# Optimization experiments

Hardware: AMD Instinct MI355X
Metric: run time of the kernel (lower is better)

## Reference

```python
import jax, jax.numpy as jnp
import numpy as np

N = 100000      # nodes
E = 1600000     # edges
D = 64          # in_dim (node/edge feature dim)
H = 128         # hidden = 2*in_dim (num_layers=2 MLP)
OUT = 64        # out_dim
EPS = 1e-7      # GENConv eps
BN_EPS = 1e-5   # BatchNorm1d eps
NORM_EPS = 1e-12  # F.normalize eps


def setup_inputs() -> dict:
    key = jax.random.key(0)
    ks = jax.random.split(key, 10)
    feats = jax.random.normal(ks[0], (N, D), dtype=jnp.float32)
    edge_h = jax.random.normal(ks[1], (E, D), dtype=jnp.float32)
    src = jax.random.randint(ks[2], (E,), 0, N, dtype=jnp.int32)
    dst = jax.random.randint(ks[3], (E,), 0, N, dtype=jnp.int32)
    # MLP params: Linear(D,H) -> BN(H) -> ReLU -> Linear(H,OUT)
    W1 = jax.random.normal(ks[4], (D, H), dtype=jnp.float32) * 0.05
    b1 = jnp.zeros((H,), dtype=jnp.float32)
    gamma = jnp.ones((H,), dtype=jnp.float32)
    bn_beta = jnp.zeros((H,), dtype=jnp.float32)
    W2 = jax.random.normal(ks[5], (H, OUT), dtype=jnp.float32) * 0.05
    b2 = jnp.zeros((OUT,), dtype=jnp.float32)
    scale = jnp.ones((1,), dtype=jnp.float32)  # MessageNorm scale (not learned)
    return {"feats": feats, "edge_h": edge_h, "src": src, "dst": dst,
            "W1": W1, "b1": b1, "gamma": gamma, "bn_beta": bn_beta,
            "W2": W2, "b2": b2, "scale": scale}


def reference(feats, edge_h, W1, b1, gamma, bn_beta, W2, b2, scale, src, dst):
    beta = 1.0
    # message: m = relu(x_src + e) + eps            [E, D]
    m = jax.nn.relu(feats[src] + edge_h) + EPS
    # edge_softmax over incoming edges of each dst node (per feature channel)
    logits = m * beta
    gmax = jax.ops.segment_max(logits, dst, num_segments=N)   # [N, D]
    ex = jnp.exp(logits - gmax[dst])                          # [E, D]
    den = jax.ops.segment_sum(ex, dst, num_segments=N)        # [N, D]
    a = ex / den[dst]
    # weighted scatter-sum aggregation
    h = jax.ops.segment_sum(m * a, dst, num_segments=N)       # [N, D]
    # MessageNorm: feats + normalize(msg) * ||feats||_2 * scale
    feat_norm = jnp.linalg.norm(feats, axis=-1, keepdims=True)
    msg_norm = jnp.linalg.norm(h, axis=-1, keepdims=True)
    msg = h / jnp.maximum(msg_norm, NORM_EPS)
    x = feats + msg * feat_norm * scale
    # MLP: Linear -> BatchNorm1d (training-mode batch stats) -> ReLU -> Linear
    x = x @ W1 + b1
    mean = jnp.mean(x, axis=0)
    var = jnp.mean(jnp.square(x - mean), axis=0)  # biased, as torch BN
    x = (x - mean) * jax.lax.rsqrt(var + BN_EPS) * gamma + bn_beta
    x = jax.nn.relu(x)
    return x @ W2 + b2
```

## Files before the change

### kernel.cpp

```cpp
#include <hip/hip_runtime.h>
#include <cstdint>

#define N_NODES 100000
#define E_EDGES 1600000
#define D_IN 64
#define H_DIM 128
#define OUT_DIM 64
#define EPS_GEN 1e-7f
#define BN_EPS 1e-5f
#define NORM_EPS 1e-12f

__global__ __launch_bounds__(256) void hist_kernel(
    const int* __restrict__ dst, int* __restrict__ counts)
{
    int t = blockIdx.x * 256 + threadIdx.x;
    if (t < E_EDGES / 4) {
        int4 d = ((const int4*)dst)[t];
        atomicAdd(&counts[d.x], 1);
        atomicAdd(&counts[d.y], 1);
        atomicAdd(&counts[d.z], 1);
        atomicAdd(&counts[d.w], 1);
    }
}

__global__ __launch_bounds__(256) void scan1(
    const int* __restrict__ counts, int* __restrict__ row_start,
    int* __restrict__ bsum)
{
    __shared__ int s[256];
    int t = threadIdx.x, g = blockIdx.x * 256 + t;
    int v = (g < N_NODES) ? counts[g] : 0;
    s[t] = v;
    __syncthreads();
    #pragma unroll
    for (int off = 1; off < 256; off <<= 1) {
        int u = (t >= off) ? s[t - off] : 0;
        __syncthreads();
        s[t] += u;
        __syncthreads();
    }
    if (g < N_NODES) row_start[g] = s[t];
    if (t == 255) bsum[blockIdx.x] = s[255];
}

__global__ __launch_bounds__(512) void scan2(int* __restrict__ bsum, int nb)
{
    __shared__ int s[512];
    int t = threadIdx.x;
    int v = (t < nb) ? bsum[t] : 0;
    s[t] = v;
    __syncthreads();
    #pragma unroll
    for (int off = 1; off < 512; off <<= 1) {
        int u = (t >= off) ? s[t - off] : 0;
        __syncthreads();
        s[t] += u;
        __syncthreads();
    }
    if (t < nb) bsum[t] = s[t] - v;
}

__global__ __launch_bounds__(256) void scan3(
    const int* __restrict__ counts, const int* __restrict__ bsum,
    int* __restrict__ row_start, int* __restrict__ next)
{
    int g = blockIdx.x * 256 + threadIdx.x;
    if (g < N_NODES) {
        int incl = row_start[g];
        int rs = incl - counts[g] + bsum[blockIdx.x];
        row_start[g] = rs;
        next[g] = rs;
    }
    if (g == 0) row_start[N_NODES] = E_EDGES;
}

__global__ __launch_bounds__(256) void scatter_k(
    const int* __restrict__ dst, const int* __restrict__ src,
    int* __restrict__ next, int2* __restrict__ adj)
{
    int t = blockIdx.x * 256 + threadIdx.x;
    if (t < E_EDGES / 4) {
        int4 d = ((const int4*)dst)[t];
        int4 s = ((const int4*)src)[t];
        int e0 = 4 * t;
        int p0 = atomicAdd(&next[d.x], 1);
        adj[p0] = make_int2(e0 + 0, s.x);
        int p1 = atomicAdd(&next[d.y], 1);
        adj[p1] = make_int2(e0 + 1, s.y);
        int p2 = atomicAdd(&next[d.z], 1);
        adj[p2] = make_int2(e0 + 2, s.z);
        int p3 = atomicAdd(&next[d.w], 1);
        adj[p3] = make_int2(e0 + 3, s.w);
    }
}

__global__ __launch_bounds__(256) void aggregate(
    const float* __restrict__ feats, const float* __restrict__ edge_h,
    const int2* __restrict__ adj, const int* __restrict__ row_start,
    const float* __restrict__ scale, float* __restrict__ x)
{
    int node = blockIdx.x * 4 + (threadIdx.x >> 6);
    int lane = threadIdx.x & 63;
    if (node >= N_NODES) return;
    int rs = row_start[node], re = row_start[node + 1];
    float den = 0.f, hn = 0.f;

    for (int base = rs; base < re; base += 64) {
        int rem = min(64, re - base);
        int2 ad = (base + lane < re) ? adj[base + lane] : make_int2(0, 0);
        for (int j = 0; j < rem; j += 8) {
            #pragma unroll
            for (int u = 0; u < 8; u++) {
                int jj = j + u;
                int eid = __shfl(ad.x, jj);
                int sid = __shfl(ad.y, jj);
                float fv = feats[(size_t)sid * D_IN + lane];
                float ev = __builtin_nontemporal_load(
                               &edge_h[(size_t)eid * D_IN + lane]);
                float m = fmaxf(fv + ev, 0.f) + EPS_GEN;
                float ex = __expf(m);
                bool ok = jj < rem;
                den += ok ? ex : 0.f;
                hn  += ok ? m * ex : 0.f;
            }
        }
    }

    float h = den > 0.f ? hn / den : 0.f;
    float f = feats[(size_t)node * D_IN + lane];
    float s1 = h * h, s2 = f * f;
    #pragma unroll
    for (int off = 32; off > 0; off >>= 1) {
        s1 += __shfl_xor(s1, off, 64);
        s2 += __shfl_xor(s2, off, 64);
    }
    float xv = f + (h / fmaxf(sqrtf(s1), NORM_EPS)) * sqrtf(s2) * scale[0];
    x[(size_t)node * D_IN + lane] = xv;
}

__global__ __launch_bounds__(256) void gemm1_stats(
    const float* __restrict__ x, const float* __restrict__ W1,
    const float* __restrict__ b1, float* __restrict__ y1,
    float* __restrict__ stats)
{
    __shared__ float wlds[D_IN * H_DIM];
    __shared__ float ssum[H_DIM], ssq[H_DIM];
    int tid = threadIdx.x;
    {
        const float4* wg = (const float4*)W1;
        float4* wl = (float4*)wlds;
        #pragma unroll
        for (int i = 0; i < 8; i++) wl[tid + i * 256] = wg[tid + i * 256];
    }
    if (tid < H_DIM) { ssum[tid] = 0.f; ssq[tid] = 0.f; }
    __syncthreads();

    int rg = tid >> 5, cg = tid & 31;
    int r0 = blockIdx.x * 32 + rg * 4;
    int c0 = cg * 4;
    float acc[4][4];
    {
        float4 bb = *(const float4*)(b1 + c0);
        #pragma unroll
        for (int i = 0; i < 4; i++) {
            acc[i][0] = bb.x; acc[i][1] = bb.y; acc[i][2] = bb.z; acc[i][3] = bb.w;
        }
    }
    #pragma unroll 2
    for (int kc = 0; kc < D_IN; kc += 4) {
        float4 xr[4];
        #pragma unroll
        for (int i = 0; i < 4; i++) {
            int r = r0 + i;
            xr[i] = (r < N_NODES) ? *(const float4*)(x + (size_t)r * D_IN + kc)
                                  : make_float4(0.f, 0.f, 0.f, 0.f);
        }
        #pragma unroll
        for (int kk = 0; kk < 4; kk++) {
            float4 w4 = *(const float4*)&wlds[(kc + kk) * H_DIM + c0];
            #pragma unroll
            for (int i = 0; i < 4; i++) {
                float xv = ((const float*)&xr[i])[kk];
                acc[i][0] = fmaf(xv, w4.x, acc[i][0]);
                acc[i][1] = fmaf(xv, w4.y, acc[i][1]);
                acc[i][2] = fmaf(xv, w4.z, acc[i][2]);
                acc[i][3] = fmaf(xv, w4.w, acc[i][3]);
            }
        }
    }
    float cs[4] = {0.f, 0.f, 0.f, 0.f}, cq[4] = {0.f, 0.f, 0.f, 0.f};
    #pragma unroll
    for (int i = 0; i < 4; i++) {
        int r = r0 + i;
        if (r < N_NODES) {
            *(float4*)(y1 + (size_t)r * H_DIM + c0) =
                make_float4(acc[i][0], acc[i][1], acc[i][2], acc[i][3]);
            #pragma unroll
            for (int j = 0; j < 4; j++) {
                cs[j] += acc[i][j];
                cq[j] += acc[i][j] * acc[i][j];
            }
        }
    }
    #pragma unroll
    for (int j = 0; j < 4; j++) {
        atomicAdd(&ssum[c0 + j], cs[j]);
        atomicAdd(&ssq[c0 + j], cq[j]);
    }
    __syncthreads();
    if (tid < H_DIM) {
        unsafeAtomicAdd(&stats[tid], ssum[tid]);
        unsafeAtomicAdd(&stats[H_DIM + tid], ssq[tid]);
    }
}

__global__ __launch_bounds__(256) void gemm2_bn(
    const float* __restrict__ y1, const float* __restrict__ W2,
    const float* __restrict__ b2, const float* __restrict__ stats,
    const float* __restrict__ gamma, const float* __restrict__ beta,
    float* __restrict__ out)
{
    __shared__ float wlds[H_DIM * OUT_DIM];
    __shared__ float sc[H_DIM], sh[H_DIM];
    int tid = threadIdx.x;
    {
        const float4* wg = (const float4*)W2;
        float4* wl = (float4*)wlds;
        #pragma unroll
        for (int i = 0; i < 8; i++) wl[tid + i * 256] = wg[tid + i * 256];
    }
    if (tid < H_DIM) {
        float mean = stats[tid] * (1.f / N_NODES);
        float var  = stats[H_DIM + tid] * (1.f / N_NODES) - mean * mean;
        float rs   = rsqrtf(var + BN_EPS);
        float s    = gamma[tid] * rs;
        sc[tid] = s;
        sh[tid] = beta[tid] - mean * s;
    }
    __syncthreads();

    int rg = tid >> 4, cg = tid & 15;
    int r0 = blockIdx.x * 64 + rg * 4;
    int c0 = cg * 4;
    float acc[4][4];
    {
        float4 bb = *(const float4*)(b2 + c0);
        #pragma unroll
        for (int i = 0; i < 4; i++) {
            acc[i][0] = bb.x; acc[i][1] = bb.y; acc[i][2] = bb.z; acc[i][3] = bb.w;
        }
    }
    #pragma unroll 2
    for (int kc = 0; kc < H_DIM; kc += 4) {
        float4 sc4 = *(const float4*)&sc[kc];
        float4 sh4 = *(const float4*)&sh[kc];
        float4 yr[4];
        #pragma unroll
        for (int i = 0; i < 4; i++) {
            int r = r0 + i;
            if (r < N_NODES) {
                float4 v = *(const float4*)(y1 + (size_t)r * H_DIM + kc);
                v.x = fmaxf(fmaf(v.x, sc4.x, sh4.x), 0.f);
                v.y = fmaxf(fmaf(v.y, sc4.y, sh4.y), 0.f);
                v.z = fmaxf(fmaf(v.z, sc4.z, sh4.z), 0.f);
                v.w = fmaxf(fmaf(v.w, sc4.w, sh4.w), 0.f);
                yr[i] = v;
            } else {
                yr[i] = make_float4(0.f, 0.f, 0.f, 0.f);
            }
        }
        #pragma unroll
        for (int kk = 0; kk < 4; kk++) {
            float4 w4 = *(const float4*)&wlds[(kc + kk) * OUT_DIM + c0];
            #pragma unroll
            for (int i = 0; i < 4; i++) {
                float yv = ((const float*)&yr[i])[kk];
                acc[i][0] = fmaf(yv, w4.x, acc[i][0]);
                acc[i][1] = fmaf(yv, w4.y, acc[i][1]);
                acc[i][2] = fmaf(yv, w4.z, acc[i][2]);
                acc[i][3] = fmaf(yv, w4.w, acc[i][3]);
            }
        }
    }
    #pragma unroll
    for (int i = 0; i < 4; i++) {
        int r = r0 + i;
        if (r < N_NODES) {
            *(float4*)(out + (size_t)r * OUT_DIM + c0) =
                make_float4(acc[i][0], acc[i][1], acc[i][2], acc[i][3]);
        }
    }
}

extern "C" void kernel_launch(void* const* d_in, const int* in_sizes, int n_in,
                              void* d_out, int out_size, void* d_ws, size_t ws_size,
                              hipStream_t stream)
{
    const float* feats   = (const float*)d_in[0];
    const float* edge_h  = (const float*)d_in[1];
    const int*   src     = (const int*)d_in[2];
    const int*   dst     = (const int*)d_in[3];
    const float* W1      = (const float*)d_in[4];
    const float* b1      = (const float*)d_in[5];
    const float* gamma   = (const float*)d_in[6];
    const float* bn_beta = (const float*)d_in[7];
    const float* W2      = (const float*)d_in[8];
    const float* b2      = (const float*)d_in[9];
    const float* scale   = (const float*)d_in[10];
    float* out = (float*)d_out;

    const size_t ND = (size_t)N_NODES * D_IN;
    char* ws = (char*)d_ws;
    int*   counts    = (int*)ws;                          ws += (size_t)N_NODES * 4;
    float* stats     = (float*)ws;                        ws += 256 * 4;
    int*   bsum      = (int*)ws;                          ws += 512 * 4;
    int*   row_start = (int*)ws;                          ws += (size_t)(N_NODES + 1) * 4;
    int*   next      = (int*)ws;                          ws += (size_t)(N_NODES + 1) * 4;
    int2*  adj       = (int2*)ws;                         ws += (size_t)E_EDGES * 8;
    float* xbuf      = (float*)ws;                        ws += ND * 4;
    float* y1        = (float*)ws;

    const int NB = (N_NODES + 255) / 256;
    const int EB4 = (E_EDGES / 4 + 255) / 256;

    hipMemsetAsync(counts, 0, (size_t)(N_NODES + 256) * 4, stream);

    hist_kernel<<<EB4, 256, 0, stream>>>(dst, counts);
    scan1<<<NB, 256, 0, stream>>>(counts, row_start, bsum);
    scan2<<<1, 512, 0, stream>>>(bsum, NB);
    scan3<<<NB, 256, 0, stream>>>(counts, bsum, row_start, next);
    scatter_k<<<EB4, 256, 0, stream>>>(dst, src, next, adj);
    aggregate<<<(N_NODES + 3) / 4, 256, 0, stream>>>(feats, edge_h, adj, row_start, scale, xbuf);
    gemm1_stats<<<(N_NODES + 31) / 32, 256, 0, stream>>>(xbuf, W1, b1, y1, stats);
    gemm2_bn<<<(N_NODES + 63) / 64, 256, 0, stream>>>(y1, W2, b2, stats, gamma, bn_beta, out);
}
```

Baseline: 965.7 us.

## Replace CSR build and gather aggregation with per-edge float atomic scatter

Drops the histogram, three-pass scan and adjacency scatter that built a CSR by destination. Each wave now handles 8 edges, computes exp(m) and m*exp(m) directly, and adds them into per-node den/hn buffers with unsafe float atomics. A separate finalize kernel divides and applies the message norm. The max subtraction is skipped (it was already absent before), which matters because m >= 0 and exp is unbounded. The cost is 2*E*D float atomics to global memory and nondeterministic summation order, in exchange for removing the preprocessing kernels and the random adj reads.

```diff
diff --git a/kernel.cpp b/kernel.cpp
--- a/kernel.cpp
+++ b/kernel.cpp
@@ -10,132 +10,60 @@
 #define BN_EPS 1e-5f
 #define NORM_EPS 1e-12f
 
-__global__ __launch_bounds__(256) void hist_kernel(
-    const int* __restrict__ dst, int* __restrict__ counts)
-{
-    int t = blockIdx.x * 256 + threadIdx.x;
-    if (t < E_EDGES / 4) {
-        int4 d = ((const int4*)dst)[t];
-        atomicAdd(&counts[d.x], 1);
-        atomicAdd(&counts[d.y], 1);
-        atomicAdd(&counts[d.z], 1);
-        atomicAdd(&counts[d.w], 1);
-    }
-}
-
-__global__ __launch_bounds__(256) void scan1(
-    const int* __restrict__ counts, int* __restrict__ row_start,
-    int* __restrict__ bsum)
-{
-    __shared__ int s[256];
-    int t = threadIdx.x, g = blockIdx.x * 256 + t;
-    int v = (g < N_NODES) ? counts[g] : 0;
-    s[t] = v;
-    __syncthreads();
-    #pragma unroll
-    for (int off = 1; off < 256; off <<= 1) {
-        int u = (t >= off) ? s[t - off] : 0;
-        __syncthreads();
-        s[t] += u;
-        __syncthreads();
-    }
-    if (g < N_NODES) row_start[g] = s[t];
-    if (t == 255) bsum[blockIdx.x] = s[255];
-}
-
-__global__ __launch_bounds__(512) void scan2(int* __restrict__ bsum, int nb)
-{
-    __shared__ int s[512];
-    int t = threadIdx.x;
-    int v = (t < nb) ? bsum[t] : 0;
-    s[t] = v;
-    __syncthreads();
-    #pragma unroll
-    for (int off = 1; off < 512; off <<= 1) {
-        int u = (t >= off) ? s[t - off] : 0;
-        __syncthreads();
-        s[t] += u;
-        __syncthreads();
-    }
-    if (t < nb) bsum[t] = s[t] - v;
-}
-
-__global__ __launch_bounds__(256) void scan3(
-    const int* __restrict__ counts, const int* __restrict__ bsum,
-    int* __restrict__ row_start, int* __restrict__ next)
-{
-    int g = blockIdx.x * 256 + threadIdx.x;
-    if (g < N_NODES) {
-        int incl = row_start[g];
-        int rs = incl - counts[g] + bsum[blockIdx.x];
-        row_start[g] = rs;
-        next[g] = rs;
-    }
-    if (g == 0) row_start[N_NODES] = E_EDGES;
-}
-
-__global__ __launch_bounds__(256) void scatter_k(
+
+__global__ __launch_bounds__(256) void edge_atomic(
     const int* __restrict__ dst, const int* __restrict__ src,
-    int* __restrict__ next, int2* __restrict__ adj)
-{
-    int t = blockIdx.x * 256 + threadIdx.x;
-    if (t < E_EDGES / 4) {
-        int4 d = ((const int4*)dst)[t];
-        int4 s = ((const int4*)src)[t];
-        int e0 = 4 * t;
-        int p0 = atomicAdd(&next[d.x], 1);
-        adj[p0] = make_int2(e0 + 0, s.x);
-        int p1 = atomicAdd(&next[d.y], 1);
-        adj[p1] = make_int2(e0 + 1, s.y);
-        int p2 = atomicAdd(&next[d.z], 1);
-        adj[p2] = make_int2(e0 + 2, s.z);
-        int p3 = atomicAdd(&next[d.w], 1);
-        adj[p3] = make_int2(e0 + 3, s.w);
-    }
-}
-
-__global__ __launch_bounds__(256) void aggregate(
     const float* __restrict__ feats, const float* __restrict__ edge_h,
-    const int2* __restrict__ adj, const int* __restrict__ row_start,
-    const float* __restrict__ scale, float* __restrict__ x)
+    float* __restrict__ den, float* __restrict__ hn)
+{
+    int wid  = blockIdx.x * 4 + (threadIdx.x >> 6);
+    int lane = threadIdx.x & 63;
+    int e0 = wid * 8;
+    int d_l = 0, s_l = 0;
+    if (lane < 8) {
+        d_l = dst[e0 + lane];
+        s_l = src[e0 + lane];
+    }
+    float ev[8], fv[8];
+    int   du[8];
+    #pragma unroll
+    for (int u = 0; u < 8; u++) {
+        du[u] = __shfl(d_l, u);
+        int su = __shfl(s_l, u);
+        ev[u] = __builtin_nontemporal_load(
+                    &edge_h[(size_t)(e0 + u) * D_IN + lane]);
+        fv[u] = feats[(size_t)su * D_IN + lane];
+    }
+    #pragma unroll
+    for (int u = 0; u < 8; u++) {
+        float m  = fmaxf(fv[u] + ev[u], 0.f) + EPS_GEN;
+        float ex = __expf(m);
+        size_t off = (size_t)du[u] * D_IN + lane;
+        unsafeAtomicAdd(&den[off], ex);
+        unsafeAtomicAdd(&hn[off], m * ex);
+    }
+}
+
+__global__ __launch_bounds__(256) void finalize_x(
+    const float* __restrict__ feats, const float* __restrict__ den,
+    const float* __restrict__ hn, const float* __restrict__ scale,
+    float* __restrict__ x)
 {
     int node = blockIdx.x * 4 + (threadIdx.x >> 6);
     int lane = threadIdx.x & 63;
     if (node >= N_NODES) return;
-    int rs = row_start[node], re = row_start[node + 1];
-    float den = 0.f, hn = 0.f;
-
-    for (int base = rs; base < re; base += 64) {
-        int rem = min(64, re - base);
-        int2 ad = (base + lane < re) ? adj[base + lane] : make_int2(0, 0);
-        for (int j = 0; j < rem; j += 8) {
-            #pragma unroll
-            for (int u = 0; u < 8; u++) {
-                int jj = j + u;
-                int eid = __shfl(ad.x, jj);
-                int sid = __shfl(ad.y, jj);
-                float fv = feats[(size_t)sid * D_IN + lane];
-                float ev = __builtin_nontemporal_load(
-                               &edge_h[(size_t)eid * D_IN + lane]);
-                float m = fmaxf(fv + ev, 0.f) + EPS_GEN;
-                float ex = __expf(m);
-                bool ok = jj < rem;
-                den += ok ? ex : 0.f;
-                hn  += ok ? m * ex : 0.f;
-            }
-        }
-    }
-
-    float h = den > 0.f ? hn / den : 0.f;
-    float f = feats[(size_t)node * D_IN + lane];
+    size_t off = (size_t)node * D_IN + lane;
+    float dv = den[off];
+    float h  = dv > 0.f ? hn[off] / dv : 0.f;
+    float f  = feats[off];
     float s1 = h * h, s2 = f * f;
     #pragma unroll
-    for (int off = 32; off > 0; off >>= 1) {
-        s1 += __shfl_xor(s1, off, 64);
-        s2 += __shfl_xor(s2, off, 64);
+    for (int o = 32; o > 0; o >>= 1) {
+        s1 += __shfl_xor(s1, o, 64);
+        s2 += __shfl_xor(s2, o, 64);
     }
     float xv = f + (h / fmaxf(sqrtf(s1), NORM_EPS)) * sqrtf(s2) * scale[0];
-    x[(size_t)node * D_IN + lane] = xv;
+    x[off] = xv;
 }
 
 __global__ __launch_bounds__(256) void gemm1_stats(
@@ -311,26 +239,16 @@
 
     const size_t ND = (size_t)N_NODES * D_IN;
     char* ws = (char*)d_ws;
-    int*   counts    = (int*)ws;                          ws += (size_t)N_NODES * 4;
-    float* stats     = (float*)ws;                        ws += 256 * 4;
-    int*   bsum      = (int*)ws;                          ws += 512 * 4;
-    int*   row_start = (int*)ws;                          ws += (size_t)(N_NODES + 1) * 4;
-    int*   next      = (int*)ws;                          ws += (size_t)(N_NODES + 1) * 4;
-    int2*  adj       = (int2*)ws;                         ws += (size_t)E_EDGES * 8;
-    float* xbuf      = (float*)ws;                        ws += ND * 4;
-    float* y1        = (float*)ws;
-
-    const int NB = (N_NODES + 255) / 256;
-    const int EB4 = (E_EDGES / 4 + 255) / 256;
-
-    hipMemsetAsync(counts, 0, (size_t)(N_NODES + 256) * 4, stream);
-
-    hist_kernel<<<EB4, 256, 0, stream>>>(dst, counts);
-    scan1<<<NB, 256, 0, stream>>>(counts, row_start, bsum);
-    scan2<<<1, 512, 0, stream>>>(bsum, NB);
-    scan3<<<NB, 256, 0, stream>>>(counts, bsum, row_start, next);
-    scatter_k<<<EB4, 256, 0, stream>>>(dst, src, next, adj);
-    aggregate<<<(N_NODES + 3) / 4, 256, 0, stream>>>(feats, edge_h, adj, row_start, scale, xbuf);
+    float* den   = (float*)ws;                            ws += ND * 4;
+    float* hn    = (float*)ws;                            ws += ND * 4;
+    float* stats = (float*)ws;                            ws += 256 * 4;
+    float* xbuf  = (float*)ws;                            ws += ND * 4;
+    float* y1    = (float*)ws;
+
+    hipMemsetAsync(den, 0, (ND * 2 + 256) * 4, stream);
+
+    edge_atomic<<<E_EDGES / 32, 256, 0, stream>>>(dst, src, feats, edge_h, den, hn);
+    finalize_x<<<(N_NODES + 3) / 4, 256, 0, stream>>>(feats, den, hn, scale, xbuf);
     gemm1_stats<<<(N_NODES + 31) / 32, 256, 0, stream>>>(xbuf, W1, b1, y1, stats);
     gemm2_bn<<<(N_NODES + 63) / 64, 256, 0, stream>>>(y1, W2, b2, stats, gamma, bn_beta, out);
 }
```

After: 1.285 ms. +33.0%, slower.
